# Kernel optimization log

Measured on AMD Instinct MI355X. Metric: run time of the kernel, lower is better.

Reference implementation:

```python
import jax, jax.numpy as jnp
import numpy as np

B = 64        # number of queries (eg_idx groups)
EPQ = 2048    # edges per query (contiguous blocks, sorted by eg_idx)
E = B * EPQ   # 131072 total edges
D = 128       # n_dims_in; G3 dim = 4*D = 512
N = 50000     # number of visited nodes
K = 256       # max_edges (top-k per query)


def setup_inputs() -> dict:
    key = jax.random.key(0)
    ks = jax.random.split(key, 9)
    scale = np.sqrt(2.0 / (4 * D)).astype(np.float32)
    return {
        "visited_node_score": jax.random.uniform(ks[0], (N,), jnp.float32),
        "visited_node_representation": jax.random.normal(ks[1], (N, D), jnp.float32),
        "rel_emb": jax.random.normal(ks[2], (E, D), jnp.float32),
        "query_src_ts_emb": jax.random.normal(ks[3], (B, D), jnp.float32),
        "query_rel_emb": jax.random.normal(ks[4], (B, D), jnp.float32),
        "Wq": jax.random.normal(ks[5], (4 * D, 4 * D), jnp.float32) * scale,
        "Wk": jax.random.normal(ks[6], (4 * D, 4 * D), jnp.float32) * scale,
        # sorted eg_idx with exactly EPQ edges per query -> regular per-group topk
        "eg_idx": (jnp.arange(E) // EPQ).astype(jnp.int32),
        "node_idx_i": jax.random.randint(ks[7], (E,), 0, N, jnp.int32),
        "node_idx_j": jax.random.randint(ks[8], (E,), 0, N, jnp.int32),
        "k": K,
    }


def segment_softmax(logits, seg, num_segments):
    # numerically-stable softmax over edges sharing the same source node
    m = jax.ops.segment_max(logits, seg, num_segments=num_segments)
    m = jax.lax.stop_gradient(m)
    ex = jnp.exp(logits - m[seg])
    s = jax.ops.segment_sum(ex, seg, num_segments=num_segments)
    return ex / s[seg]


def reference(visited_node_score, visited_node_representation, rel_emb,
              query_src_ts_emb, query_rel_emb, Wq, Wk,
              eg_idx, node_idx_i, node_idx_j, k):
    # gather node / query embeddings per edge (torch index_select)
    hvi = visited_node_representation[node_idx_i]          # [E, D]
    hvj = visited_node_representation[node_idx_j]          # [E, D]
    qs = query_src_ts_emb[eg_idx]                          # [E, D]
    qr = query_rel_emb[eg_idx]                             # [E, D]
    # G3 bilinear: sum(query_proj(cat(left)) * key_proj(cat(right)), -1)
    left = jnp.concatenate([hvi, rel_emb, qs, qr], axis=-1)   # [E, 4D]
    right = jnp.concatenate([hvj, rel_emb, qs, qr], axis=-1)  # [E, 4D]
    logits = jnp.sum((left @ Wq.T) * (right @ Wk.T), axis=-1) # [E]
    # softmax over edges grouped by source node idx (edges[:, -2])
    attn = segment_softmax(logits, node_idx_i, N)              # [E]
    src_score = visited_node_score[node_idx_i]                 # [E]
    target_score = attn * src_score                            # [E]
    # per-query top-k pruning (each query owns a contiguous EPQ block, EPQ > k)
    top_vals, top_idx = jax.lax.top_k(target_score.reshape(B, EPQ), k)
    flat_idx = (top_idx + jnp.arange(B, dtype=top_idx.dtype)[:, None] * EPQ).reshape(-1)
    pruned_attn = attn[flat_idx]                # transition_logits_pruned_softmax
    pruned_src = src_score[flat_idx]            # pruned_src_score
    pruned_tgt = node_idx_j[flat_idx]           # pruned_edges[:, 7]
    # 'sum' node score aggregation: sparse mm == segment_sum of attn * src_score
    updated_node_score = jax.ops.segment_sum(pruned_attn * pruned_src,
                                             pruned_tgt, num_segments=N)
    return updated_node_score
```

## Files before the change

kernel.cpp:

```cpp
#include <hip/hip_runtime.h>
#include <cstddef>

#define EPQ_SHIFT 11
#define KSEL 256

typedef __attribute__((ext_vector_type(8))) short short8v;
typedef __attribute__((ext_vector_type(4))) float float4v;

__device__ __forceinline__ unsigned enc_f(float f) {
  unsigned u = __float_as_uint(f);
  return (u & 0x80000000u) ? ~u : (u | 0x80000000u);
}
__device__ __forceinline__ float dec_f(unsigned k) {
  unsigned u = (k & 0x80000000u) ? (k ^ 0x80000000u) : ~k;
  return __uint_as_float(u);
}
__device__ __forceinline__ unsigned short f2bf(float x) {
  unsigned u = __float_as_uint(x);
  return (unsigned short)((u + 0x7FFFu + ((u >> 16) & 1u)) >> 16);
}

__global__ void k0_init(float* __restrict__ out, float* __restrict__ segsum,
                        unsigned* __restrict__ segkey, int n) {
  int i = blockIdx.x * 256 + threadIdx.x;
  if (i < n) { out[i] = 0.f; segsum[i] = 0.f; segkey[i] = 0u; }
}

__global__ __launch_bounds__(256) void k1_gemmM(
    const float* __restrict__ Wq, const float* __restrict__ Wk,
    float* __restrict__ M, float* __restrict__ Mt,
    unsigned short* __restrict__ Mh, unsigned short* __restrict__ Ml,
    unsigned short* __restrict__ Mth, unsigned short* __restrict__ Mtl) {
  __shared__ float as[16][64];
  __shared__ float bs[16][64];
  int tid = threadIdx.x;
  int tx = tid & 15, ty = tid >> 4;
  int c1b = blockIdx.y * 64, c2b = blockIdx.x * 64;
  float acc[4][4] = {};
  for (int k0 = 0; k0 < 512; k0 += 16) {
#pragma unroll
    for (int l = 0; l < 4; ++l) {
      int lin = tid + l * 256;
      int kk = lin >> 6, c = lin & 63;
      as[kk][c] = Wq[(k0 + kk) * 512 + c1b + c];
      bs[kk][c] = Wk[(k0 + kk) * 512 + c2b + c];
    }
    __syncthreads();
#pragma unroll
    for (int kk = 0; kk < 16; ++kk) {
      float a[4], b[4];
#pragma unroll
      for (int m = 0; m < 4; ++m) a[m] = as[kk][ty * 4 + m];
#pragma unroll
      for (int n = 0; n < 4; ++n) b[n] = bs[kk][tx * 4 + n];
#pragma unroll
      for (int m = 0; m < 4; ++m)
#pragma unroll
        for (int n = 0; n < 4; ++n) acc[m][n] += a[m] * b[n];
    }
    __syncthreads();
  }
#pragma unroll
  for (int m = 0; m < 4; ++m)
#pragma unroll
    for (int n = 0; n < 4; ++n) {
      int c1 = c1b + ty * 4 + m, c2 = c2b + tx * 4 + n;
      float v = acc[m][n];
      M[c1 * 512 + c2] = v;
      Mt[c2 * 512 + c1] = v;
      unsigned short h = f2bf(v);
      unsigned short lo = f2bf(v - __uint_as_float((unsigned)h << 16));
      Mh[c1 * 512 + c2] = h;
      Ml[c1 * 512 + c2] = lo;
      Mth[c2 * 512 + c1] = h;
      Mtl[c2 * 512 + c1] = lo;
    }
}

#define STAGE_A_F32(SRC_PTR)                                                 \
  {                                                                          \
    const float* s = (SRC_PTR);                                              \
    float4 v0 = *(const float4*)&s[0];                                       \
    float4 v1 = *(const float4*)&s[4];                                       \
    float4 v2 = *(const float4*)&s[8];                                       \
    float4 v3 = *(const float4*)&s[12];                                      \
    float vv[16] = {v0.x, v0.y, v0.z, v0.w, v1.x, v1.y, v1.z, v1.w,          \
                    v2.x, v2.y, v2.z, v2.w, v3.x, v3.y, v3.z, v3.w};         \
    unsigned hw[8], lw[8];                                                   \
    _Pragma("unroll") for (int j = 0; j < 8; ++j) {                          \
      unsigned short h0 = f2bf(vv[2 * j]);                                   \
      unsigned short h1 = f2bf(vv[2 * j + 1]);                               \
      unsigned short l0 =                                                    \
          f2bf(vv[2 * j] - __uint_as_float((unsigned)h0 << 16));             \
      unsigned short l1 =                                                    \
          f2bf(vv[2 * j + 1] - __uint_as_float((unsigned)h1 << 16));         \
      hw[j] = (unsigned)h0 | ((unsigned)h1 << 16);                           \
      lw[j] = (unsigned)l0 | ((unsigned)l1 << 16);                           \
    }                                                                        \
    int sw = (sn >> 1) & 3;                                                  \
    int g0 = (shalf * 2) ^ sw, g1 = (shalf * 2 + 1) ^ sw;                    \
    *(uint4*)&Ah[sn][g0 * 8] = make_uint4(hw[0], hw[1], hw[2], hw[3]);       \
    *(uint4*)&Ah[sn][g1 * 8] = make_uint4(hw[4], hw[5], hw[6], hw[7]);       \
    *(uint4*)&Al[sn][g0 * 8] = make_uint4(lw[0], lw[1], lw[2], lw[3]);       \
    *(uint4*)&Al[sn][g1 * 8] = make_uint4(lw[4], lw[5], lw[6], lw[7]);       \
  }

#define STAGE_B_BF16(HSRC, LSRC)                                             \
  {                                                                          \
    const unsigned short* sh_ = (HSRC);                                      \
    const unsigned short* sl_ = (LSRC);                                      \
    uint4 q0 = *(const uint4*)&sh_[0];                                       \
    uint4 q1 = *(const uint4*)&sh_[8];                                       \
    uint4 p0 = *(const uint4*)&sl_[0];                                       \
    uint4 p1 = *(const uint4*)&sl_[8];                                       \
    int sw = (sn >> 1) & 3;                                                  \
    int g0 = (shalf * 2) ^ sw, g1 = (shalf * 2 + 1) ^ sw;                    \
    *(uint4*)&Bh[sn][g0 * 8] = q0;                                           \
    *(uint4*)&Bh[sn][g1 * 8] = q1;                                           \
    *(uint4*)&Bl[sn][g0 * 8] = p0;                                           \
    *(uint4*)&Bl[sn][g1 * 8] = p1;                                           \
  }

#define MFMA_CHUNK()                                                         \
  {                                                                          \
    int ln = lane & 15, kq = lane >> 4;                                      \
    short8v ah[4], al[4];                                                    \
    _Pragma("unroll") for (int r = 0; r < 4; ++r) {                          \
      int row = wr2 * 64 + r * 16 + ln;                                      \
      int gg = kq ^ ((row >> 1) & 3);                                        \
      ah[r] = *(const short8v*)&Ah[row][gg * 8];                             \
      al[r] = *(const short8v*)&Al[row][gg * 8];                             \
    }                                                                        \
    _Pragma("unroll") for (int c = 0; c < 4; ++c) {                          \
      int col = wc2 * 64 + c * 16 + ln;                                      \
      int gg = kq ^ ((col >> 1) & 3);                                        \
      short8v bh = *(const short8v*)&Bh[col][gg * 8];                        \
      short8v bl = *(const short8v*)&Bl[col][gg * 8];                        \
      _Pragma("unroll") for (int r = 0; r < 4; ++r) {                        \
        acc[r][c] = __builtin_amdgcn_mfma_f32_16x16x32_bf16(                 \
            ah[r], bh, acc[r][c], 0, 0, 0);                                  \
        acc[r][c] = __builtin_amdgcn_mfma_f32_16x16x32_bf16(                 \
            ah[r], bl, acc[r][c], 0, 0, 0);                                  \
        acc[r][c] = __builtin_amdgcn_mfma_f32_16x16x32_bf16(                 \
            al[r], bh, acc[r][c], 0, 0, 0);                                  \
      }                                                                      \
    }                                                                        \
  }

__global__ __launch_bounds__(256) void k2m_mfma(
    const float* __restrict__ hv, const unsigned short* __restrict__ Mh,
    const unsigned short* __restrict__ Ml, const unsigned short* __restrict__ Mth,
    const unsigned short* __restrict__ Mtl, float* __restrict__ J0,
    float* __restrict__ J1, float* __restrict__ I1, int N) {
  __shared__ char pool[32768];
  unsigned short (*Ah)[32] = (unsigned short(*)[32])pool;
  unsigned short (*Al)[32] = (unsigned short(*)[32])(pool + 8192);
  unsigned short (*Bh)[32] = (unsigned short(*)[32])(pool + 16384);
  unsigned short (*Bl)[32] = (unsigned short(*)[32])(pool + 24576);
  float (*ep)[34] = (float(*)[34])pool;

  const int tid = threadIdx.x;
  const int lane = tid & 63;
  const int w = tid >> 6;
  const int wr2 = w >> 1, wc2 = w & 1;
  const int p = blockIdx.x;
  const int n0 = blockIdx.y * 128;
  const unsigned short* bhs = (p == 2) ? Mth : Mh;
  const unsigned short* bls = (p == 2) ? Mtl : Ml;
  const int rowoff = (p == 0) ? 0 : 128;
  float* outp = (p == 0) ? J0 : (p == 1) ? J1 : I1;

  float4v acc[4][4];
#pragma unroll
  for (int r = 0; r < 4; ++r)
#pragma unroll
    for (int c = 0; c < 4; ++c) acc[r][c] = (float4v){0.f, 0.f, 0.f, 0.f};

  const int sn = tid >> 1, shalf = tid & 1;
  for (int ch = 0; ch < 4; ++ch) {
    __syncthreads();
    {
      int gn = n0 + sn;
      gn = gn < N ? gn : N - 1;
      STAGE_A_F32(hv + (size_t)gn * 128 + ch * 32 + shalf * 16);
      size_t boff = (size_t)(rowoff + sn) * 512 + ch * 32 + shalf * 16;
      STAGE_B_BF16(bhs + boff, bls + boff);
    }
    __syncthreads();
    MFMA_CHUNK();
  }

  for (int g = 0; g < 4; ++g) {
    __syncthreads();
    if (wc2 == (g >> 1)) {
      int ln = lane & 15, kq = lane >> 4;
#pragma unroll
      for (int cc = 0; cc < 2; ++cc) {
        int c = (g & 1) * 2 + cc;
#pragma unroll
        for (int r = 0; r < 4; ++r)
#pragma unroll
          for (int reg = 0; reg < 4; ++reg)
            ep[wr2 * 64 + r * 16 + kq * 4 + reg][cc * 16 + ln] = acc[r][c][reg];
      }
    }
    __syncthreads();
    int row = tid >> 1, half = tid & 1;
    int gn = n0 + row;
    if (gn < N) {
#pragma unroll
      for (int j = 0; j < 4; ++j)
        *(float4*)&outp[(size_t)gn * 128 + 32 * g + 16 * half + 4 * j] =
            *(const float4*)&ep[row][16 * half + 4 * j];
    }
  }
}

__global__ __launch_bounds__(128) void k3_query(const float* __restrict__ qsrc,
                                                const float* __restrict__ qrel,
                                                const float* __restrict__ M,
                                                const float* __restrict__ Mt,
                                                float* __restrict__ wv,
                                                float* __restrict__ uv,
                                                float* __restrict__ yv,
                                                float* __restrict__ cb) {
  __shared__ float qcat[256];
  __shared__ float red[128];
  int b = blockIdx.x, d = threadIdx.x;
  qcat[d] = qsrc[b * 128 + d];
  qcat[128 + d] = qrel[b * 128 + d];
  __syncthreads();
  float w = 0.f, u = 0.f, y = 0.f, t1 = 0.f, t2 = 0.f;
  for (int c = 0; c < 256; ++c) {
    float q = qcat[c];
    size_t row = (size_t)(256 + c) * 512;
    w += Mt[row + d] * q;
    u += M[row + d] * q;
    y += (Mt[row + 128 + d] + M[row + 128 + d]) * q;
    t1 += M[row + 256 + d] * q;
    t2 += M[row + 384 + d] * q;
  }
  wv[b * 128 + d] = w;
  uv[b * 128 + d] = u;
  yv[b * 128 + d] = y;
  red[d] = qcat[d] * t1 + qcat[128 + d] * t2;
  __syncthreads();
  for (int s = 64; s > 0; s >>= 1) {
    if (d < s) red[d] += red[d + s];
    __syncthreads();
  }
  if (d == 0) cb[b] = red[0];
}

__global__ __launch_bounds__(256) void k4m_mfma(
    const float* __restrict__ rel, const unsigned short* __restrict__ Mth,
    const unsigned short* __restrict__ Mtl, const float* __restrict__ yv,
    const float* __restrict__ cbp, float* __restrict__ ec) {
  __shared__ char pool[32768];
  unsigned short (*Ah)[32] = (unsigned short(*)[32])pool;
  unsigned short (*Al)[32] = (unsigned short(*)[32])(pool + 8192);
  unsigned short (*Bh)[32] = (unsigned short(*)[32])(pool + 16384);
  unsigned short (*Bl)[32] = (unsigned short(*)[32])(pool + 24576);
  float (*ep)[34] = (float(*)[34])pool;

  const int tid = threadIdx.x;
  const int lane = tid & 63;
  const int w = tid >> 6;
  const int wr2 = w >> 1, wc2 = w & 1;
  const int e0 = blockIdx.x * 128;
  const int b = e0 >> EPQ_SHIFT;

  float4v acc[4][4];
#pragma unroll
  for (int r = 0; r < 4; ++r)
#pragma unroll
    for (int c = 0; c < 4; ++c) acc[r][c] = (float4v){0.f, 0.f, 0.f, 0.f};

  const int sn = tid >> 1, shalf = tid & 1;
  for (int ch = 0; ch < 4; ++ch) {
    __syncthreads();
    {
      STAGE_A_F32(rel + (size_t)(e0 + sn) * 128 + ch * 32 + shalf * 16);
      size_t boff = (size_t)(128 + sn) * 512 + 128 + ch * 32 + shalf * 16;
      STAGE_B_BF16(Mth + boff, Mtl + boff);
    }
    __syncthreads();
    MFMA_CHUNK();
  }

  float part = 0.f;
  const int e_loc = tid >> 1, half = tid & 1;
  for (int g = 0; g < 4; ++g) {
    __syncthreads();
    if (wc2 == (g >> 1)) {
      int ln = lane & 15, kq = lane >> 4;
#pragma unroll
      for (int cc = 0; cc < 2; ++cc) {
        int c = (g & 1) * 2 + cc;
#pragma unroll
        for (int r = 0; r < 4; ++r)
#pragma unroll
          for (int reg = 0; reg < 4; ++reg)
            ep[wr2 * 64 + r * 16 + kq * 4 + reg][cc * 16 + ln] = acc[r][c][reg];
      }
    }
    __syncthreads();
    const float* rsrc = rel + (size_t)(e0 + e_loc) * 128 + 32 * g + 16 * half;
    const float* ysrc = yv + b * 128 + 32 * g + 16 * half;
#pragma unroll
    for (int j = 0; j < 4; ++j) {
      float4 q = *(const float4*)&ep[e_loc][16 * half + 4 * j];
      float4 rr = *(const float4*)&rsrc[4 * j];
      float4 yy = *(const float4*)&ysrc[4 * j];
      part += (q.x + yy.x) * rr.x + (q.y + yy.y) * rr.y +
              (q.z + yy.z) * rr.z + (q.w + yy.w) * rr.w;
    }
  }
  part += __shfl_xor(part, 1, 64);
  if ((tid & 1) == 0) ec[e0 + e_loc] = part + cbp[b];
}

__global__ __launch_bounds__(256) void k5_logits(const float* __restrict__ rel,
                                                 const float* __restrict__ hv,
                                                 const float* __restrict__ J0,
                                                 const float* __restrict__ J1,
                                                 const float* __restrict__ I1,
                                                 const float* __restrict__ wv,
                                                 const float* __restrict__ uv,
                                                 const float* __restrict__ ec,
                                                 const int* __restrict__ node_i,
                                                 const int* __restrict__ node_j,
                                                 float* __restrict__ logits,
                                                 unsigned* __restrict__ segkey) {
  __shared__ float wl[128];
  __shared__ float ul[128];
  int tid = threadIdx.x;
  int e0 = blockIdx.x * 16;
  int b = e0 >> EPQ_SHIFT;
  if (tid < 128) wl[tid] = wv[b * 128 + tid];
  else ul[tid - 128] = uv[b * 128 + (tid - 128)];
  __syncthreads();
  int lane = tid & 15, eg = tid >> 4;
  int e = e0 + eg;
  int i = node_i[e], j = node_j[e];
  int c0 = lane * 8;

  float rr[8], hi[8], hj[8], a0[8], a1[8], ii[8];
  *(float4*)&rr[0] = *(const float4*)&rel[(size_t)e * 128 + c0];
  *(float4*)&rr[4] = *(const float4*)&rel[(size_t)e * 128 + c0 + 4];
  *(float4*)&hi[0] = *(const float4*)&hv[(size_t)i * 128 + c0];
  *(float4*)&hi[4] = *(const float4*)&hv[(size_t)i * 128 + c0 + 4];
  *(float4*)&hj[0] = *(const float4*)&hv[(size_t)j * 128 + c0];
  *(float4*)&hj[4] = *(const float4*)&hv[(size_t)j * 128 + c0 + 4];
  *(float4*)&a0[0] = *(const float4*)&J0[(size_t)j * 128 + c0];
  *(float4*)&a0[4] = *(const float4*)&J0[(size_t)j * 128 + c0 + 4];
  *(float4*)&a1[0] = *(const float4*)&J1[(size_t)j * 128 + c0];
  *(float4*)&a1[4] = *(const float4*)&J1[(size_t)j * 128 + c0 + 4];
  *(float4*)&ii[0] = *(const float4*)&I1[(size_t)i * 128 + c0];
  *(float4*)&ii[4] = *(const float4*)&I1[(size_t)i * 128 + c0 + 4];

  float p = 0.f;
#pragma unroll
  for (int k = 0; k < 8; ++k) {
    p += hi[k] * a0[k];
    p += rr[k] * (a1[k] + ii[k]);
    p += hi[k] * wl[c0 + k];
    p += hj[k] * ul[c0 + k];
  }
#pragma unroll
  for (int m = 8; m >= 1; m >>= 1) p += __shfl_xor(p, m, 64);
  if (lane == 0) {
    float lg = p + ec[e];
    logits[e] = lg;
    atomicMax(&segkey[i], enc_f(lg));
  }
}

__global__ void k6_exp(float* __restrict__ exb, const int* __restrict__ node_i,
                       const unsigned* __restrict__ segkey,
                       float* __restrict__ segsum, int E) {
  int e = blockIdx.x * 256 + threadIdx.x;
  if (e >= E) return;
  int i = node_i[e];
  float m = dec_f(segkey[i]);
  float ex = expf(exb[e] - m);
  exb[e] = ex;
  atomicAdd(&segsum[i], ex);
}

__global__ __launch_bounds__(256) void k7_topk(const float* __restrict__ exb,
                                               const int* __restrict__ node_i,
                                               const int* __restrict__ node_j,
                                               const float* __restrict__ segsum,
                                               const float* __restrict__ score,
                                               float* __restrict__ out) {
  __shared__ unsigned vals[2048];
  __shared__ unsigned hist[256];
  __shared__ unsigned sc[256];
  __shared__ unsigned tie_scan[256];
  __shared__ unsigned sel_info[2];
  int q = blockIdx.x, t = threadIdx.x;
  size_t base = (size_t)q * 2048;
#pragma unroll
  for (int l = 0; l < 8; ++l) {
    int el = t * 8 + l;
    int i = node_i[base + el];
    float tgt = exb[base + el] / segsum[i] * score[i];
    vals[el] = __float_as_uint(tgt);
  }
  __syncthreads();
  unsigned prefix = 0, need = KSEL;
  for (int pass = 3; pass >= 0; --pass) {
    hist[t] = 0;
    __syncthreads();
    int sh = pass * 8;
#pragma unroll
    for (int l = 0; l < 8; ++l) {
      unsigned v = vals[t * 8 + l];
      bool match = (pass == 3) || ((v >> (sh + 8)) == (prefix >> (sh + 8)));
      if (match) atomicAdd(&hist[(v >> sh) & 255u], 1u);
    }
    __syncthreads();
    sc[t] = hist[t];
    __syncthreads();
    for (int off = 1; off < 256; off <<= 1) {
      unsigned add = (t + off < 256) ? sc[t + off] : 0u;
      __syncthreads();
      sc[t] += add;
      __syncthreads();
    }
    unsigned above = sc[t] - hist[t];
    if (above < need && need <= sc[t]) {
      sel_info[0] = (unsigned)t;
      sel_info[1] = need - above;
    }
    __syncthreads();
    prefix |= sel_info[0] << sh;
    need = sel_info[1];
    __syncthreads();
  }
  unsigned T = prefix, r = need;
  unsigned lc = 0;
#pragma unroll
  for (int l = 0; l < 8; ++l)
    if (vals[t * 8 + l] == T) lc++;
  tie_scan[t] = lc;
  __syncthreads();
  unsigned own = lc;
  for (int off = 1; off < 256; off <<= 1) {
    unsigned add = (t >= off) ? tie_scan[t - off] : 0u;
    __syncthreads();
    tie_scan[t] += add;
    __syncthreads();
  }
  unsigned excl = tie_scan[t] - own;
  unsigned cnt = 0;
#pragma unroll
  for (int l = 0; l < 8; ++l) {
    int el = t * 8 + l;
    unsigned v = vals[el];
    bool take = false;
    if (v > T) take = true;
    else if (v == T) { if (excl + cnt < r) take = true; cnt++; }
    if (take) {
      int j = node_j[base + el];
      atomicAdd(&out[j], __uint_as_float(v));
    }
  }
}

extern "C" void kernel_launch(void* const* d_in, const int* in_sizes, int n_in,
                              void* d_out, int out_size, void* d_ws, size_t ws_size,
                              hipStream_t stream) {
  const float* score = (const float*)d_in[0];
  const float* hv    = (const float*)d_in[1];
  const float* rel   = (const float*)d_in[2];
  const float* qsrc  = (const float*)d_in[3];
  const float* qrel  = (const float*)d_in[4];
  const float* Wq    = (const float*)d_in[5];
  const float* Wk    = (const float*)d_in[6];
  const int* node_i  = (const int*)d_in[8];
  const int* node_j  = (const int*)d_in[9];

  const int N = in_sizes[0];
  const int B = in_sizes[3] / 128;
  const int E = in_sizes[2] / 128;

  float* ws = (float*)d_ws;
  float* M  = ws;
  float* Mt = M + 262144;
  float* J0 = Mt + 262144;
  float* J1 = J0 + (size_t)N * 128;
  float* I1 = J1 + (size_t)N * 128;
  float* wv = I1 + (size_t)N * 128;
  float* uv = wv + (size_t)B * 128;
  float* yv = uv + (size_t)B * 128;
  float* cb = yv + (size_t)B * 128;
  float* ec = cb + B;
  float* exb = ec + E;
  unsigned* segkey = (unsigned*)(exb + E);
  float* segsum = (float*)(segkey + N);
  unsigned short* Mh  = (unsigned short*)(segsum + N);
  unsigned short* Ml  = Mh + 262144;
  unsigned short* Mth = Ml + 262144;
  unsigned short* Mtl = Mth + 262144;
  float* out = (float*)d_out;

  k0_init<<<(N + 255) / 256, 256, 0, stream>>>(out, segsum, segkey, N);
  k1_gemmM<<<dim3(8, 8), 256, 0, stream>>>(Wq, Wk, M, Mt, Mh, Ml, Mth, Mtl);
  k2m_mfma<<<dim3(3, (N + 127) / 128), 256, 0, stream>>>(hv, Mh, Ml, Mth, Mtl,
                                                         J0, J1, I1, N);
  k3_query<<<B, 128, 0, stream>>>(qsrc, qrel, M, Mt, wv, uv, yv, cb);
  k4m_mfma<<<E / 128, 256, 0, stream>>>(rel, Mth, Mtl, yv, cb, ec);
  k5_logits<<<E / 16, 256, 0, stream>>>(rel, hv, J0, J1, I1, wv, uv, ec,
                                        node_i, node_j, exb, segkey);
  k6_exp<<<(E + 255) / 256, 256, 0, stream>>>(exb, node_i, segkey, segsum, E);
  k7_topk<<<B, 256, 0, stream>>>(exb, node_i, node_j, segsum, score, out);
}
```

Baseline: 228.1 us.

## Fuse edge-constant and logits kernels, interleave J0/J1 layout, fold init into GEMM

Merges the per-edge constant MFMA kernel with the gather-based logits kernel, so the edge constant stays in shared memory and no longer takes a global round trip or a separate launch. J0 and J1 are stored interleaved in one 256-wide row so each gathered node j reads one contiguous region. The zero-init kernel is folded into the M GEMM kernel, and the query kernel splits its reduction across 256 threads. The logits phase now uses two lanes per edge with 64 columns each, which changes memory-level parallelism and register use compared with the previous 16 lanes per edge.

```diff
diff --git a/kernel.cpp b/kernel.cpp
--- a/kernel.cpp
+++ b/kernel.cpp
@@ -18,22 +18,26 @@
 __device__ __forceinline__ unsigned short f2bf(float x) {
   unsigned u = __float_as_uint(x);
   return (unsigned short)((u + 0x7FFFu + ((u >> 16) & 1u)) >> 16);
-}
-
-__global__ void k0_init(float* __restrict__ out, float* __restrict__ segsum,
-                        unsigned* __restrict__ segkey, int n) {
-  int i = blockIdx.x * 256 + threadIdx.x;
-  if (i < n) { out[i] = 0.f; segsum[i] = 0.f; segkey[i] = 0u; }
 }
 
 __global__ __launch_bounds__(256) void k1_gemmM(
     const float* __restrict__ Wq, const float* __restrict__ Wk,
     float* __restrict__ M, float* __restrict__ Mt,
     unsigned short* __restrict__ Mh, unsigned short* __restrict__ Ml,
-    unsigned short* __restrict__ Mth, unsigned short* __restrict__ Mtl) {
+    unsigned short* __restrict__ Mth, unsigned short* __restrict__ Mtl,
+    float* __restrict__ outz, float* __restrict__ segsum,
+    unsigned* __restrict__ segkey, int N) {
+  int tid = threadIdx.x;
+  {
+    int bid = blockIdx.y * gridDim.x + blockIdx.x;
+    for (int idx = bid * 256 + tid; idx < N; idx += 16384) {
+      outz[idx] = 0.f;
+      segsum[idx] = 0.f;
+      segkey[idx] = 0u;
+    }
+  }
   __shared__ float as[16][64];
   __shared__ float bs[16][64];
-  int tid = threadIdx.x;
   int tx = tid & 15, ty = tid >> 4;
   int c1b = blockIdx.y * 64, c2b = blockIdx.x * 64;
   float acc[4][4] = {};
@@ -150,8 +154,8 @@
 __global__ __launch_bounds__(256) void k2m_mfma(
     const float* __restrict__ hv, const unsigned short* __restrict__ Mh,
     const unsigned short* __restrict__ Ml, const unsigned short* __restrict__ Mth,
-    const unsigned short* __restrict__ Mtl, float* __restrict__ J0,
-    float* __restrict__ J1, float* __restrict__ I1, int N) {
+    const unsigned short* __restrict__ Mtl, float* __restrict__ Tj,
+    float* __restrict__ I1, int N) {
   __shared__ char pool[32768];
   unsigned short (*Ah)[32] = (unsigned short(*)[32])pool;
   unsigned short (*Al)[32] = (unsigned short(*)[32])(pool + 8192);
@@ -168,7 +172,8 @@
   const unsigned short* bhs = (p == 2) ? Mth : Mh;
   const unsigned short* bls = (p == 2) ? Mtl : Ml;
   const int rowoff = (p == 0) ? 0 : 128;
-  float* outp = (p == 0) ? J0 : (p == 1) ? J1 : I1;
+  float* outp = (p == 0) ? Tj : (p == 1) ? (Tj + 128) : I1;
+  const size_t ostride = (p == 2) ? 128 : 256;
 
   float4v acc[4][4];
 #pragma unroll
@@ -210,13 +215,13 @@
     if (gn < N) {
 #pragma unroll
       for (int j = 0; j < 4; ++j)
-        *(float4*)&outp[(size_t)gn * 128 + 32 * g + 16 * half + 4 * j] =
+        *(float4*)&outp[(size_t)gn * ostride + 32 * g + 16 * half + 4 * j] =
             *(const float4*)&ep[row][16 * half + 4 * j];
     }
   }
 }
 
-__global__ __launch_bounds__(128) void k3_query(const float* __restrict__ qsrc,
+__global__ __launch_bounds__(256) void k3_query(const float* __restrict__ qsrc,
                                                 const float* __restrict__ qrel,
                                                 const float* __restrict__ M,
                                                 const float* __restrict__ Mt,
@@ -225,13 +230,14 @@
                                                 float* __restrict__ yv,
                                                 float* __restrict__ cb) {
   __shared__ float qcat[256];
+  __shared__ float prt[5][256];
   __shared__ float red[128];
-  int b = blockIdx.x, d = threadIdx.x;
-  qcat[d] = qsrc[b * 128 + d];
-  qcat[128 + d] = qrel[b * 128 + d];
+  int b = blockIdx.x, tid = threadIdx.x;
+  int d = tid & 127, hc = tid >> 7;
+  qcat[tid] = (tid < 128) ? qsrc[b * 128 + tid] : qrel[b * 128 + (tid - 128)];
   __syncthreads();
   float w = 0.f, u = 0.f, y = 0.f, t1 = 0.f, t2 = 0.f;
-  for (int c = 0; c < 256; ++c) {
+  for (int c = hc * 128; c < hc * 128 + 128; ++c) {
     float q = qcat[c];
     size_t row = (size_t)(256 + c) * 512;
     w += Mt[row + d] * q;
@@ -240,28 +246,45 @@
     t1 += M[row + 256 + d] * q;
     t2 += M[row + 384 + d] * q;
   }
-  wv[b * 128 + d] = w;
-  uv[b * 128 + d] = u;
-  yv[b * 128 + d] = y;
-  red[d] = qcat[d] * t1 + qcat[128 + d] * t2;
+  prt[0][tid] = w; prt[1][tid] = u; prt[2][tid] = y;
+  prt[3][tid] = t1; prt[4][tid] = t2;
+  __syncthreads();
+  if (tid < 128) {
+    float wc_ = prt[0][d] + prt[0][128 + d];
+    float uc = prt[1][d] + prt[1][128 + d];
+    float yc = prt[2][d] + prt[2][128 + d];
+    float t1c = prt[3][d] + prt[3][128 + d];
+    float t2c = prt[4][d] + prt[4][128 + d];
+    wv[b * 128 + d] = wc_;
+    uv[b * 128 + d] = uc;
+    yv[b * 128 + d] = yc;
+    red[d] = qcat[d] * t1c + qcat[128 + d] * t2c;
+  }
   __syncthreads();
   for (int s = 64; s > 0; s >>= 1) {
-    if (d < s) red[d] += red[d + s];
-    __syncthreads();
-  }
-  if (d == 0) cb[b] = red[0];
-}
-
-__global__ __launch_bounds__(256) void k4m_mfma(
+    if (tid < s) red[tid] += red[tid + s];
+    __syncthreads();
+  }
+  if (tid == 0) cb[b] = red[0];
+}
+
+__global__ __launch_bounds__(256) void k45_fused(
     const float* __restrict__ rel, const unsigned short* __restrict__ Mth,
     const unsigned short* __restrict__ Mtl, const float* __restrict__ yv,
-    const float* __restrict__ cbp, float* __restrict__ ec) {
+    const float* __restrict__ cbp, const float* __restrict__ hv,
+    const float* __restrict__ Tj, const float* __restrict__ I1,
+    const int* __restrict__ node_i, const int* __restrict__ node_j,
+    const float* __restrict__ wvv, const float* __restrict__ uvv,
+    float* __restrict__ logits, unsigned* __restrict__ segkey) {
   __shared__ char pool[32768];
   unsigned short (*Ah)[32] = (unsigned short(*)[32])pool;
   unsigned short (*Al)[32] = (unsigned short(*)[32])(pool + 8192);
   unsigned short (*Bh)[32] = (unsigned short(*)[32])(pool + 16384);
   unsigned short (*Bl)[32] = (unsigned short(*)[32])(pool + 24576);
   float (*ep)[34] = (float(*)[34])pool;
+  __shared__ float ecl[128];
+  __shared__ float wl[128];
+  __shared__ float ul[128];
 
   const int tid = threadIdx.x;
   const int lane = tid & 63;
@@ -270,6 +293,9 @@
   const int e0 = blockIdx.x * 128;
   const int b = e0 >> EPQ_SHIFT;
 
+  if (tid < 128) wl[tid] = wvv[b * 128 + tid];
+  else ul[tid - 128] = uvv[b * 128 + (tid - 128)];
+
   float4v acc[4][4];
 #pragma unroll
   for (int r = 0; r < 4; ++r)
@@ -289,7 +315,7 @@
   }
 
   float part = 0.f;
-  const int e_loc = tid >> 1, half = tid & 1;
+  const int e_loc1 = tid >> 1, half1 = tid & 1;
   for (int g = 0; g < 4; ++g) {
     __syncthreads();
     if (wc2 == (g >> 1)) {
@@ -305,11 +331,11 @@
       }
     }
     __syncthreads();
-    const float* rsrc = rel + (size_t)(e0 + e_loc) * 128 + 32 * g + 16 * half;
-    const float* ysrc = yv + b * 128 + 32 * g + 16 * half;
+    const float* rsrc = rel + (size_t)(e0 + e_loc1) * 128 + 32 * g + 16 * half1;
+    const float* ysrc = yv + b * 128 + 32 * g + 16 * half1;
 #pragma unroll
     for (int j = 0; j < 4; ++j) {
-      float4 q = *(const float4*)&ep[e_loc][16 * half + 4 * j];
+      float4 q = *(const float4*)&ep[e_loc1][16 * half1 + 4 * j];
       float4 rr = *(const float4*)&rsrc[4 * j];
       float4 yy = *(const float4*)&ysrc[4 * j];
       part += (q.x + yy.x) * rr.x + (q.y + yy.y) * rr.y +
@@ -317,62 +343,44 @@
     }
   }
   part += __shfl_xor(part, 1, 64);
-  if ((tid & 1) == 0) ec[e0 + e_loc] = part + cbp[b];
-}
-
-__global__ __launch_bounds__(256) void k5_logits(const float* __restrict__ rel,
-                                                 const float* __restrict__ hv,
-                                                 const float* __restrict__ J0,
-                                                 const float* __restrict__ J1,
-                                                 const float* __restrict__ I1,
-                                                 const float* __restrict__ wv,
-                                                 const float* __restrict__ uv,
-                                                 const float* __restrict__ ec,
-                                                 const int* __restrict__ node_i,
-                                                 const int* __restrict__ node_j,
-                                                 float* __restrict__ logits,
-                                                 unsigned* __restrict__ segkey) {
-  __shared__ float wl[128];
-  __shared__ float ul[128];
-  int tid = threadIdx.x;
-  int e0 = blockIdx.x * 16;
-  int b = e0 >> EPQ_SHIFT;
-  if (tid < 128) wl[tid] = wv[b * 128 + tid];
-  else ul[tid - 128] = uv[b * 128 + (tid - 128)];
+  if ((tid & 1) == 0) ecl[e_loc1] = part + cbp[b];
   __syncthreads();
-  int lane = tid & 15, eg = tid >> 4;
-  int e = e0 + eg;
-  int i = node_i[e], j = node_j[e];
-  int c0 = lane * 8;
-
-  float rr[8], hi[8], hj[8], a0[8], a1[8], ii[8];
-  *(float4*)&rr[0] = *(const float4*)&rel[(size_t)e * 128 + c0];
-  *(float4*)&rr[4] = *(const float4*)&rel[(size_t)e * 128 + c0 + 4];
-  *(float4*)&hi[0] = *(const float4*)&hv[(size_t)i * 128 + c0];
-  *(float4*)&hi[4] = *(const float4*)&hv[(size_t)i * 128 + c0 + 4];
-  *(float4*)&hj[0] = *(const float4*)&hv[(size_t)j * 128 + c0];
-  *(float4*)&hj[4] = *(const float4*)&hv[(size_t)j * 128 + c0 + 4];
-  *(float4*)&a0[0] = *(const float4*)&J0[(size_t)j * 128 + c0];
-  *(float4*)&a0[4] = *(const float4*)&J0[(size_t)j * 128 + c0 + 4];
-  *(float4*)&a1[0] = *(const float4*)&J1[(size_t)j * 128 + c0];
-  *(float4*)&a1[4] = *(const float4*)&J1[(size_t)j * 128 + c0 + 4];
-  *(float4*)&ii[0] = *(const float4*)&I1[(size_t)i * 128 + c0];
-  *(float4*)&ii[4] = *(const float4*)&I1[(size_t)i * 128 + c0 + 4];
-
-  float p = 0.f;
-#pragma unroll
-  for (int k = 0; k < 8; ++k) {
-    p += hi[k] * a0[k];
-    p += rr[k] * (a1[k] + ii[k]);
-    p += hi[k] * wl[c0 + k];
-    p += hj[k] * ul[c0 + k];
-  }
-#pragma unroll
-  for (int m = 8; m >= 1; m >>= 1) p += __shfl_xor(p, m, 64);
-  if (lane == 0) {
-    float lg = p + ec[e];
-    logits[e] = lg;
-    atomicMax(&segkey[i], enc_f(lg));
+
+  {
+    const int eslot = lane >> 1, half = lane & 1;
+    const int e_loc = w * 32 + eslot;
+    const int e = e0 + e_loc;
+    const int i = node_i[e], j = node_j[e];
+    const int c0 = half * 64;
+    const float* relp = rel + (size_t)e * 128 + c0;
+    const float* hvi = hv + (size_t)i * 128 + c0;
+    const float* hvj = hv + (size_t)j * 128 + c0;
+    const float* tjp = Tj + (size_t)j * 256 + c0;
+    const float* iip = I1 + (size_t)i * 128 + c0;
+
+    float p = 0.f;
+#pragma unroll
+    for (int k = 0; k < 16; ++k) {
+      float4 rr = *(const float4*)&relp[4 * k];
+      float4 h_i = *(const float4*)&hvi[4 * k];
+      float4 h_j = *(const float4*)&hvj[4 * k];
+      float4 a0 = *(const float4*)&tjp[4 * k];
+      float4 a1 = *(const float4*)&tjp[128 + 4 * k];
+      float4 ii = *(const float4*)&iip[4 * k];
+      float4 w4 = *(const float4*)&wl[c0 + 4 * k];
+      float4 u4 = *(const float4*)&ul[c0 + 4 * k];
+      p += h_i.x * a0.x + h_i.y * a0.y + h_i.z * a0.z + h_i.w * a0.w;
+      p += rr.x * (a1.x + ii.x) + rr.y * (a1.y + ii.y) +
+           rr.z * (a1.z + ii.z) + rr.w * (a1.w + ii.w);
+      p += h_i.x * w4.x + h_i.y * w4.y + h_i.z * w4.z + h_i.w * w4.w;
+      p += h_j.x * u4.x + h_j.y * u4.y + h_j.z * u4.z + h_j.w * u4.w;
+    }
+    p += __shfl_xor(p, 1, 64);
+    if (half == 0) {
+      float lg = p + ecl[e_loc];
+      logits[e] = lg;
+      atomicMax(&segkey[i], enc_f(lg));
+    }
   }
 }
 
@@ -489,15 +497,13 @@
   float* ws = (float*)d_ws;
   float* M  = ws;
   float* Mt = M + 262144;
-  float* J0 = Mt + 262144;
-  float* J1 = J0 + (size_t)N * 128;
-  float* I1 = J1 + (size_t)N * 128;
+  float* Tj = Mt + 262144;
+  float* I1 = Tj + (size_t)N * 256;
   float* wv = I1 + (size_t)N * 128;
   float* uv = wv + (size_t)B * 128;
   float* yv = uv + (size_t)B * 128;
   float* cb = yv + (size_t)B * 128;
-  float* ec = cb + B;
-  float* exb = ec + E;
+  float* exb = cb + B;
   unsigned* segkey = (unsigned*)(exb + E);
   float* segsum = (float*)(segkey + N);
   unsigned short* Mh  = (unsigned short*)(segsum + N);
@@ -506,14 +512,13 @@
   unsigned short* Mtl = Mth + 262144;
   float* out = (float*)d_out;
 
-  k0_init<<<(N + 255) / 256, 256, 0, stream>>>(out, segsum, segkey, N);
-  k1_gemmM<<<dim3(8, 8), 256, 0, stream>>>(Wq, Wk, M, Mt, Mh, Ml, Mth, Mtl);
+  k1_gemmM<<<dim3(8, 8), 256, 0, stream>>>(Wq, Wk, M, Mt, Mh, Ml, Mth, Mtl,
+                                           out, segsum, segkey, N);
   k2m_mfma<<<dim3(3, (N + 127) / 128), 256, 0, stream>>>(hv, Mh, Ml, Mth, Mtl,
-                                                         J0, J1, I1, N);
-  k3_query<<<B, 128, 0, stream>>>(qsrc, qrel, M, Mt, wv, uv, yv, cb);
-  k4m_mfma<<<E / 128, 256, 0, stream>>>(rel, Mth, Mtl, yv, cb, ec);
-  k5_logits<<<E / 16, 256, 0, stream>>>(rel, hv, J0, J1, I1, wv, uv, ec,
-                                        node_i, node_j, exb, segkey);
+                                                         Tj, I1, N);
+  k3_query<<<B, 256, 0, stream>>>(qsrc, qrel, M, Mt, wv, uv, yv, cb);
+  k45_fused<<<E / 128, 256, 0, stream>>>(rel, Mth, Mtl, yv, cb, hv, Tj, I1,
+                                         node_i, node_j, wv, uv, exb, segkey);
   k6_exp<<<(E + 255) / 256, 256, 0, stream>>>(exb, node_i, segkey, segsum, E);
   k7_topk<<<B, 256, 0, stream>>>(exb, node_i, node_j, segsum, score, out);
 }
```

Result: slower. 322.7 us (+41.5%).

## Interleave J0/J1 tables, fold init into GEMM kernel, split query reduction

Applied to the files above, without the earlier changes.

Stores the two per-node tables J0 and J1 interleaved in one 256-wide row so the gather in the logits kernel fetches both from one contiguous 1 KB region per node j. The zero-initialisation kernel is folded into the weight GEMM kernel as a grid-stride loop, which saves one launch. The query kernel now uses 256 threads, each half reducing over half the channels, with a shared-memory combine step. The risks are extra shared-memory use in the query kernel and some added work at the start of each GEMM block.

```diff
diff --git a/kernel.cpp b/kernel.cpp
--- a/kernel.cpp
+++ b/kernel.cpp
@@ -18,22 +18,26 @@
 __device__ __forceinline__ unsigned short f2bf(float x) {
   unsigned u = __float_as_uint(x);
   return (unsigned short)((u + 0x7FFFu + ((u >> 16) & 1u)) >> 16);
-}
-
-__global__ void k0_init(float* __restrict__ out, float* __restrict__ segsum,
-                        unsigned* __restrict__ segkey, int n) {
-  int i = blockIdx.x * 256 + threadIdx.x;
-  if (i < n) { out[i] = 0.f; segsum[i] = 0.f; segkey[i] = 0u; }
 }
 
 __global__ __launch_bounds__(256) void k1_gemmM(
     const float* __restrict__ Wq, const float* __restrict__ Wk,
     float* __restrict__ M, float* __restrict__ Mt,
     unsigned short* __restrict__ Mh, unsigned short* __restrict__ Ml,
-    unsigned short* __restrict__ Mth, unsigned short* __restrict__ Mtl) {
+    unsigned short* __restrict__ Mth, unsigned short* __restrict__ Mtl,
+    float* __restrict__ outz, float* __restrict__ segsum,
+    unsigned* __restrict__ segkey, int N) {
+  int tid = threadIdx.x;
+  {
+    int bid = blockIdx.y * gridDim.x + blockIdx.x;
+    for (int idx = bid * 256 + tid; idx < N; idx += 16384) {
+      outz[idx] = 0.f;
+      segsum[idx] = 0.f;
+      segkey[idx] = 0u;
+    }
+  }
   __shared__ float as[16][64];
   __shared__ float bs[16][64];
-  int tid = threadIdx.x;
   int tx = tid & 15, ty = tid >> 4;
   int c1b = blockIdx.y * 64, c2b = blockIdx.x * 64;
   float acc[4][4] = {};
@@ -150,8 +154,8 @@
 __global__ __launch_bounds__(256) void k2m_mfma(
     const float* __restrict__ hv, const unsigned short* __restrict__ Mh,
     const unsigned short* __restrict__ Ml, const unsigned short* __restrict__ Mth,
-    const unsigned short* __restrict__ Mtl, float* __restrict__ J0,
-    float* __restrict__ J1, float* __restrict__ I1, int N) {
+    const unsigned short* __restrict__ Mtl, float* __restrict__ Tj,
+    float* __restrict__ I1, int N) {
   __shared__ char pool[32768];
   unsigned short (*Ah)[32] = (unsigned short(*)[32])pool;
   unsigned short (*Al)[32] = (unsigned short(*)[32])(pool + 8192);
@@ -168,7 +172,8 @@
   const unsigned short* bhs = (p == 2) ? Mth : Mh;
   const unsigned short* bls = (p == 2) ? Mtl : Ml;
   const int rowoff = (p == 0) ? 0 : 128;
-  float* outp = (p == 0) ? J0 : (p == 1) ? J1 : I1;
+  float* outp = (p == 0) ? Tj : (p == 1) ? (Tj + 128) : I1;
+  const size_t ostride = (p == 2) ? 128 : 256;
 
   float4v acc[4][4];
 #pragma unroll
@@ -210,13 +215,13 @@
     if (gn < N) {
 #pragma unroll
       for (int j = 0; j < 4; ++j)
-        *(float4*)&outp[(size_t)gn * 128 + 32 * g + 16 * half + 4 * j] =
+        *(float4*)&outp[(size_t)gn * ostride + 32 * g + 16 * half + 4 * j] =
             *(const float4*)&ep[row][16 * half + 4 * j];
     }
   }
 }
 
-__global__ __launch_bounds__(128) void k3_query(const float* __restrict__ qsrc,
+__global__ __launch_bounds__(256) void k3_query(const float* __restrict__ qsrc,
                                                 const float* __restrict__ qrel,
                                                 const float* __restrict__ M,
                                                 const float* __restrict__ Mt,
@@ -225,13 +230,14 @@
                                                 float* __restrict__ yv,
                                                 float* __restrict__ cb) {
   __shared__ float qcat[256];
+  __shared__ float prt[5][256];
   __shared__ float red[128];
-  int b = blockIdx.x, d = threadIdx.x;
-  qcat[d] = qsrc[b * 128 + d];
-  qcat[128 + d] = qrel[b * 128 + d];
+  int b = blockIdx.x, tid = threadIdx.x;
+  int d = tid & 127, hc = tid >> 7;
+  qcat[tid] = (tid < 128) ? qsrc[b * 128 + tid] : qrel[b * 128 + (tid - 128)];
   __syncthreads();
   float w = 0.f, u = 0.f, y = 0.f, t1 = 0.f, t2 = 0.f;
-  for (int c = 0; c < 256; ++c) {
+  for (int c = hc * 128; c < hc * 128 + 128; ++c) {
     float q = qcat[c];
     size_t row = (size_t)(256 + c) * 512;
     w += Mt[row + d] * q;
@@ -240,16 +246,26 @@
     t1 += M[row + 256 + d] * q;
     t2 += M[row + 384 + d] * q;
   }
-  wv[b * 128 + d] = w;
-  uv[b * 128 + d] = u;
-  yv[b * 128 + d] = y;
-  red[d] = qcat[d] * t1 + qcat[128 + d] * t2;
+  prt[0][tid] = w; prt[1][tid] = u; prt[2][tid] = y;
+  prt[3][tid] = t1; prt[4][tid] = t2;
+  __syncthreads();
+  if (tid < 128) {
+    float wc_ = prt[0][d] + prt[0][128 + d];
+    float uc = prt[1][d] + prt[1][128 + d];
+    float yc = prt[2][d] + prt[2][128 + d];
+    float t1c = prt[3][d] + prt[3][128 + d];
+    float t2c = prt[4][d] + prt[4][128 + d];
+    wv[b * 128 + d] = wc_;
+    uv[b * 128 + d] = uc;
+    yv[b * 128 + d] = yc;
+    red[d] = qcat[d] * t1c + qcat[128 + d] * t2c;
+  }
   __syncthreads();
   for (int s = 64; s > 0; s >>= 1) {
-    if (d < s) red[d] += red[d + s];
-    __syncthreads();
-  }
-  if (d == 0) cb[b] = red[0];
+    if (tid < s) red[tid] += red[tid + s];
+    __syncthreads();
+  }
+  if (tid == 0) cb[b] = red[0];
 }
 
 __global__ __launch_bounds__(256) void k4m_mfma(
@@ -322,8 +338,7 @@
 
 __global__ __launch_bounds__(256) void k5_logits(const float* __restrict__ rel,
                                                  const float* __restrict__ hv,
-                                                 const float* __restrict__ J0,
-                                                 const float* __restrict__ J1,
+                                                 const float* __restrict__ Tj,
                                                  const float* __restrict__ I1,
                                                  const float* __restrict__ wv,
                                                  const float* __restrict__ uv,
@@ -352,10 +367,10 @@
   *(float4*)&hi[4] = *(const float4*)&hv[(size_t)i * 128 + c0 + 4];
   *(float4*)&hj[0] = *(const float4*)&hv[(size_t)j * 128 + c0];
   *(float4*)&hj[4] = *(const float4*)&hv[(size_t)j * 128 + c0 + 4];
-  *(float4*)&a0[0] = *(const float4*)&J0[(size_t)j * 128 + c0];
-  *(float4*)&a0[4] = *(const float4*)&J0[(size_t)j * 128 + c0 + 4];
-  *(float4*)&a1[0] = *(const float4*)&J1[(size_t)j * 128 + c0];
-  *(float4*)&a1[4] = *(const float4*)&J1[(size_t)j * 128 + c0 + 4];
+  *(float4*)&a0[0] = *(const float4*)&Tj[(size_t)j * 256 + c0];
+  *(float4*)&a0[4] = *(const float4*)&Tj[(size_t)j * 256 + c0 + 4];
+  *(float4*)&a1[0] = *(const float4*)&Tj[(size_t)j * 256 + 128 + c0];
+  *(float4*)&a1[4] = *(const float4*)&Tj[(size_t)j * 256 + 128 + c0 + 4];
   *(float4*)&ii[0] = *(const float4*)&I1[(size_t)i * 128 + c0];
   *(float4*)&ii[4] = *(const float4*)&I1[(size_t)i * 128 + c0 + 4];
 
@@ -489,9 +504,8 @@
   float* ws = (float*)d_ws;
   float* M  = ws;
   float* Mt = M + 262144;
-  float* J0 = Mt + 262144;
-  float* J1 = J0 + (size_t)N * 128;
-  float* I1 = J1 + (size_t)N * 128;
+  float* Tj = Mt + 262144;
+  float* I1 = Tj + (size_t)N * 256;
   float* wv = I1 + (size_t)N * 128;
   float* uv = wv + (size_t)B * 128;
   float* yv = uv + (size_t)B * 128;
@@ -506,13 +520,13 @@
   unsigned short* Mtl = Mth + 262144;
   float* out = (float*)d_out;
 
-  k0_init<<<(N + 255) / 256, 256, 0, stream>>>(out, segsum, segkey, N);
-  k1_gemmM<<<dim3(8, 8), 256, 0, stream>>>(Wq, Wk, M, Mt, Mh, Ml, Mth, Mtl);
+  k1_gemmM<<<dim3(8, 8), 256, 0, stream>>>(Wq, Wk, M, Mt, Mh, Ml, Mth, Mtl,
+                                           out, segsum, segkey, N);
   k2m_mfma<<<dim3(3, (N + 127) / 128), 256, 0, stream>>>(hv, Mh, Ml, Mth, Mtl,
-                                                         J0, J1, I1, N);
-  k3_query<<<B, 128, 0, stream>>>(qsrc, qrel, M, Mt, wv, uv, yv, cb);
+                                                         Tj, I1, N);
+  k3_query<<<B, 256, 0, stream>>>(qsrc, qrel, M, Mt, wv, uv, yv, cb);
   k4m_mfma<<<E / 128, 256, 0, stream>>>(rel, Mth, Mtl, yv, cb, ec);
-  k5_logits<<<E / 16, 256, 0, stream>>>(rel, hv, J0, J1, I1, wv, uv, ec,
+  k5_logits<<<E / 16, 256, 0, stream>>>(rel, hv, Tj, I1, wv, uv, ec,
                                         node_i, node_j, exb, segkey);
   k6_exp<<<(E + 255) / 256, 256, 0, stream>>>(exb, node_i, segkey, segsum, E);
   k7_topk<<<B, 256, 0, stream>>>(exb, node_i, node_j, segsum, score, out);
```

Result: slower. 237.3 us (+4.0%).
